# Kernel optimization log

Measured on AMD Instinct MI355X. Metric: run time of the kernel, lower is better.

Reference implementation:

```python
import jax, jax.numpy as jnp
import numpy as np

DIM = 3072
HEADS = 24
HD = 128
FF = 4 * DIM
EPS = 1e-6
SCALE_SHIFT = 1.0


def _ln(x):
    # LayerNorm, elementwise_affine=False
    mu = jnp.mean(x, axis=-1, keepdims=True)
    var = jnp.mean(jnp.square(x - mu), axis=-1, keepdims=True)
    return (x - mu) * jax.lax.rsqrt(var + EPS)


def _rms(x, w):
    # RMSNorm over head_dim with learned weight
    ms = jnp.mean(jnp.square(x), axis=-1, keepdims=True)
    return x * jax.lax.rsqrt(ms + EPS) * w


def _rope(x, cos, sin):
    # x: [B,S,H,D], cos/sin: [S,D]; interleaved rotate-half (diffusers style)
    xr = x.reshape(*x.shape[:-1], -1, 2)
    x1, x2 = xr[..., 0], xr[..., 1]
    rot = jnp.stack([-x2, x1], axis=-1).reshape(x.shape)
    return x * cos[None, :, None, :] + rot * sin[None, :, None, :]


def _mod_params(temb, w, b):
    m = jax.nn.silu(temb) @ w + b  # [B, 6*DIM]
    B = m.shape[0]
    m = m.reshape(B, -1, 6).transpose(0, 2, 1).reshape(B, -1)  # reorder to 6 blocks of DIM
    return jnp.split(m, 2, axis=-1)  # mod1, mod2 each [B, 3*DIM]


def _modulate(x, mp):
    shift, scale, gate = jnp.split(mp, 3, axis=-1)
    scale = scale + SCALE_SHIFT
    return x * scale[:, None, :] + shift[:, None, :], gate[:, None, :]


def setup_inputs() -> dict:
    key = jax.random.key(0)
    ks = jax.random.split(key, 32)
    B, ST, SI = 1, 512, 1024
    S = ST + SI
    r = lambda k, shp, s=1.0: jax.random.normal(k, shp, dtype=jnp.float32) * s
    W = 0.02  # weight init scale
    ang = jax.random.uniform(ks[5], (S, HD), minval=0.0, maxval=2 * np.pi)
    inp = {
        "hidden_states": r(ks[0], (B, SI, DIM)),
        "encoder_hidden_states": r(ks[1], (B, ST, DIM)),
        "encoder_hidden_states_mask": jnp.ones((B, ST), jnp.float32),
        "temb": r(ks[2], (B, DIM)),
        "rope_cos": jnp.cos(ang),
        "rope_sin": jnp.sin(ang),
        "w_img_mod": r(ks[6], (DIM, 6 * DIM), W), "b_img_mod": r(ks[7], (6 * DIM,), W),
        "w_txt_mod": r(ks[8], (DIM, 6 * DIM), W), "b_txt_mod": r(ks[9], (6 * DIM,), W),
        "norm_q_w": jnp.ones((HD,), jnp.float32), "norm_k_w": jnp.ones((HD,), jnp.float32),
        "norm_added_q_w": jnp.ones((HD,), jnp.float32), "norm_added_k_w": jnp.ones((HD,), jnp.float32),
        "w_qkv": r(ks[10], (DIM, 3 * DIM), W), "b_qkv": r(ks[11], (3 * DIM,), W),
        "w_add_qkv": r(ks[12], (DIM, 3 * DIM), W), "b_add_qkv": r(ks[13], (3 * DIM,), W),
        "w_out": r(ks[14], (DIM, DIM), W), "b_out": r(ks[15], (DIM,), W),
        "w_add_out": r(ks[16], (DIM, DIM), W), "b_add_out": r(ks[17], (DIM,), W),
        "w_img_mlp1": r(ks[18], (DIM, FF), W), "b_img_mlp1": r(ks[19], (FF,), W),
        "w_img_mlp2": r(ks[20], (FF, DIM), W), "b_img_mlp2": r(ks[21], (DIM,), W),
        "w_txt_mlp1": r(ks[22], (DIM, FF), W), "b_txt_mlp1": r(ks[23], (FF,), W),
        "w_txt_mlp2": r(ks[24], (FF, DIM), W), "b_txt_mlp2": r(ks[25], (DIM,), W),
    }
    return inp


def reference(hidden_states, encoder_hidden_states, encoder_hidden_states_mask, temb,
              rope_cos, rope_sin,
              w_img_mod, b_img_mod, w_txt_mod, b_txt_mod,
              norm_q_w, norm_k_w, norm_added_q_w, norm_added_k_w,
              w_qkv, b_qkv, w_add_qkv, b_add_qkv,
              w_out, b_out, w_add_out, b_add_out,
              w_img_mlp1, b_img_mlp1, w_img_mlp2, b_img_mlp2,
              w_txt_mlp1, b_txt_mlp1, w_txt_mlp2, b_txt_mlp2):
    B, SI, _ = hidden_states.shape
    ST = encoder_hidden_states.shape[1]

    img_mod1, img_mod2 = _mod_params(temb, w_img_mod, b_img_mod)
    txt_mod1, txt_mod2 = _mod_params(temb, w_txt_mod, b_txt_mod)

    img_m, img_g1 = _modulate(_ln(hidden_states), img_mod1)
    txt_m, txt_g1 = _modulate(_ln(encoder_hidden_states), txt_mod1)

    # joint attention
    iq, ik, iv = jnp.split(img_m @ w_qkv + b_qkv, 3, axis=-1)
    tq, tk, tv = jnp.split(txt_m @ w_add_qkv + b_add_qkv, 3, axis=-1)
    iq = _rms(iq.reshape(B, SI, HEADS, HD), norm_q_w)
    ik = _rms(ik.reshape(B, SI, HEADS, HD), norm_k_w)
    iv = iv.reshape(B, SI, HEADS, HD)
    tq = _rms(tq.reshape(B, ST, HEADS, HD), norm_added_q_w)
    tk = _rms(tk.reshape(B, ST, HEADS, HD), norm_added_k_w)
    tv = tv.reshape(B, ST, HEADS, HD)
    q = jnp.concatenate([tq, iq], axis=1)  # [B,S,H,D], txt first
    k = jnp.concatenate([tk, ik], axis=1)
    v = jnp.concatenate([tv, iv], axis=1)
    q = _rope(q, rope_cos, rope_sin)
    k = _rope(k, rope_cos, rope_sin)
    scores = jnp.einsum('bqhd,bkhd->bhqk', q, k) / np.float32(np.sqrt(HD))
    probs = jax.nn.softmax(scores, axis=-1)
    attn = jnp.einsum('bhqk,bkhd->bqhd', probs, v).reshape(B, ST + SI, HEADS * HD)

    txt_a = attn[:, :ST] @ w_add_out + b_add_out
    img_a = attn[:, ST:] @ w_out + b_out
    hidden = hidden_states + img_g1 * img_a
    enc = encoder_hidden_states + txt_g1 * txt_a

    # fused GELU(tanh) MLPs with modulation
    img_m2, img_g2 = _modulate(_ln(hidden), img_mod2)
    img_mlp = jax.nn.gelu(img_m2 @ w_img_mlp1 + b_img_mlp1, approximate=True) @ w_img_mlp2 + b_img_mlp2
    hidden = hidden + img_g2 * img_mlp

    txt_m2, txt_g2 = _modulate(_ln(enc), txt_mod2)
    txt_mlp = jax.nn.gelu(txt_m2 @ w_txt_mlp1 + b_txt_mlp1, approximate=True) @ w_txt_mlp2 + b_txt_mlp2
    enc = enc + txt_g2 * txt_mlp

    return enc, hidden
```

## Files before the change

kernel.cpp:

```cpp
#include <hip/hip_runtime.h>

#define DIMX 3072
#define STX 512
#define SIX 1024
#define SQX 1536
#define FFX 12288

typedef __attribute__((ext_vector_type(4))) float f32x4;
typedef __attribute__((ext_vector_type(8))) __bf16 bf16x8;
typedef __attribute__((ext_vector_type(4))) int i32x4;

__device__ __forceinline__ unsigned short f2bf(float f){
  unsigned u = __builtin_bit_cast(unsigned, f);
  u += 0x7FFFu + ((u>>16)&1u);
  return (unsigned short)(u>>16);
}
__device__ __forceinline__ float bf2f(unsigned short h){
  unsigned u = ((unsigned)h)<<16;
  return __builtin_bit_cast(float, u);
}
__device__ __forceinline__ float gelu_tanh(float x){
  float x3 = x*x*x;
  float z = 0.7978845608028654f*(x + 0.044715f*x3);
  z = fminf(fmaxf(z, -15.f), 15.f);
  float e = exp2f(z*2.8853900817779268f);
  float th = (e-1.f)/(e+1.f);
  return 0.5f*x*(1.f+th);
}

__device__ __forceinline__ void gload16(const void* g, void* l){
  __builtin_amdgcn_global_load_lds(
      (const __attribute__((address_space(1))) void*)g,
      (__attribute__((address_space(3))) void*)l,
      16, 0, 0);
}


__global__ void k_silu(const float* __restrict__ temb, float* __restrict__ out){
  int i = blockIdx.x*256 + threadIdx.x;
  if(i < DIMX){
    float x = temb[i];
    out[i] = x / (1.f + exp2f(-x*1.4426950408889634f));
  }
}

__global__ void k_modinit(const float* __restrict__ b_img, const float* __restrict__ b_txt,
                          float* __restrict__ mod){
  int idx = blockIdx.x*256 + threadIdx.x;
  int mat = idx / 18432; int r = idx % 18432;
  int i = r/6, j = r%6;
  const float* b = mat ? b_txt : b_img;
  mod[mat*18432 + j*3072 + i] = b[r];
}

__global__ void k_modgemv(const float* __restrict__ w_img, const float* __restrict__ w_txt,
                          const float* __restrict__ silu_t, float* __restrict__ mod){
  int bz = blockIdx.x;
  int ks = bz & 7; bz >>= 3;
  int nc = bz % 18; int mat = bz / 18;
  const float* W = mat ? w_txt : w_img;
  __shared__ float st[384];
  int k0 = ks*384;
  for(int i = threadIdx.x; i < 384; i += 256) st[i] = silu_t[k0+i];
  __syncthreads();
  int n0 = nc*1024 + threadIdx.x*4;
  float ax=0.f, ay=0.f, az=0.f, aw=0.f;
  const float* Wp = W + (size_t)k0*18432 + n0;
  #pragma unroll 4
  for(int k=0;k<384;k++){
    float4 w = *(const float4*)(Wp + (size_t)k*18432);
    float s = st[k];
    ax += s*w.x; ay += s*w.y; az += s*w.z; aw += s*w.w;
  }
  float* md = mod + mat*18432;
  float vals[4] = {ax, ay, az, aw};
  #pragma unroll
  for(int j=0;j<4;j++){
    int n = n0+j; int i = n/6, jj = n%6;
    atomicAdd(&md[jj*3072 + i], vals[j]);
  }
}

__global__ void k_initC(float* __restrict__ out, const float* __restrict__ res,
                        const float* __restrict__ gate, const float* __restrict__ bias){
  int i = (blockIdx.x*256 + threadIdx.x)*4;
  int col = i % 3072;
  float4 r = *(const float4*)(res + i);
  float4 g = *(const float4*)(gate + col);
  float4 b = *(const float4*)(bias + col);
  float4 o = {r.x + g.x*b.x, r.y + g.y*b.y, r.z + g.z*b.z, r.w + g.w*b.w};
  *(float4*)(out + i) = o;
}

__global__ void k_f2b(const float* __restrict__ x, unsigned short* __restrict__ y, int n4){
  int i = blockIdx.x*256 + threadIdx.x;
  if(i < n4){
    float4 v = *(const float4*)(x + (size_t)i*4);
    unsigned short h0 = f2bf(v.x), h1 = f2bf(v.y), h2 = f2bf(v.z), h3 = f2bf(v.w);
    unsigned long long pk = (unsigned long long)(h0 | ((unsigned)h1<<16))
                          | ((unsigned long long)(h2 | ((unsigned)h3<<16))<<32);
    *(unsigned long long*)(y + (size_t)i*4) = pk;
  }
}

__global__ void k_lnmod(const float* __restrict__ x, const float* __restrict__ modp,
                        unsigned short* __restrict__ out){
  int row = blockIdx.x, t = threadIdx.x;
  const float* xr = x + (size_t)row*DIMX;
  float4 v0 = *(const float4*)(xr + t*4);
  float4 v1 = *(const float4*)(xr + 1024 + t*4);
  float4 v2 = *(const float4*)(xr + 2048 + t*4);
  float s  = v0.x+v0.y+v0.z+v0.w + v1.x+v1.y+v1.z+v1.w + v2.x+v2.y+v2.z+v2.w;
  float s2 = v0.x*v0.x+v0.y*v0.y+v0.z*v0.z+v0.w*v0.w
           + v1.x*v1.x+v1.y*v1.y+v1.z*v1.z+v1.w*v1.w
           + v2.x*v2.x+v2.y*v2.y+v2.z*v2.z+v2.w*v2.w;
  #pragma unroll
  for(int o=32;o>0;o>>=1){ s += __shfl_xor(s,o); s2 += __shfl_xor(s2,o); }
  __shared__ float rs_[4], rs2_[4];
  int wid = t>>6;
  if((t&63)==0){ rs_[wid]=s; rs2_[wid]=s2; }
  __syncthreads();
  float S  = rs_[0]+rs_[1]+rs_[2]+rs_[3];
  float S2 = rs2_[0]+rs2_[1]+rs2_[2]+rs2_[3];
  float mu = S*(1.f/3072.f);
  float var = S2*(1.f/3072.f) - mu*mu;
  float rstd = rsqrtf(var + 1e-6f);
  #pragma unroll
  for(int j=0;j<3;j++){
    int c = j*1024 + t*4;
    float4 sh = *(const float4*)(modp + c);
    float4 sc = *(const float4*)(modp + 3072 + c);
    float4 xv = (j==0)?v0:((j==1)?v1:v2);
    unsigned short h0 = f2bf((xv.x-mu)*rstd*(sc.x+1.f)+sh.x);
    unsigned short h1 = f2bf((xv.y-mu)*rstd*(sc.y+1.f)+sh.y);
    unsigned short h2 = f2bf((xv.z-mu)*rstd*(sc.z+1.f)+sh.z);
    unsigned short h3 = f2bf((xv.w-mu)*rstd*(sc.w+1.f)+sh.w);
    unsigned long long pk = (unsigned long long)(h0 | ((unsigned)h1<<16))
                          | ((unsigned long long)(h2 | ((unsigned)h3<<16))<<32);
    *(unsigned long long*)(out + (size_t)row*DIMX + c) = pk;
  }
}

__global__ void k_rmsrope(const unsigned short* __restrict__ qkv_txt,
                          const unsigned short* __restrict__ qkv_img,
                          const float* __restrict__ nqw, const float* __restrict__ nkw,
                          const float* __restrict__ naqw, const float* __restrict__ nakw,
                          const float* __restrict__ cosb, const float* __restrict__ sinb,
                          unsigned short* __restrict__ Q, unsigned short* __restrict__ K,
                          unsigned short* __restrict__ V){
  int s = blockIdx.x, h = blockIdx.y, t = threadIdx.x;
  bool txt = s < STX;
  const unsigned short* src = txt ? (qkv_txt + (size_t)s*9216)
                                  : (qkv_img + (size_t)(s-STX)*9216);
  const float* qw = txt ? naqw : nqw;
  const float* kw = txt ? nakw : nkw;
  int d0 = 2*t;
  float q1 = bf2f(src[h*128 + d0]),        q2 = bf2f(src[h*128 + d0 + 1]);
  float k1 = bf2f(src[3072 + h*128 + d0]), k2 = bf2f(src[3072 + h*128 + d0 + 1]);
  float v1 = bf2f(src[6144 + h*128 + d0]), v2 = bf2f(src[6144 + h*128 + d0 + 1]);
  float sq = q1*q1 + q2*q2, sk = k1*k1 + k2*k2;
  #pragma unroll
  for(int o=32;o>0;o>>=1){ sq += __shfl_xor(sq,o); sk += __shfl_xor(sk,o); }
  float rq = rsqrtf(sq*(1.f/128.f) + 1e-6f);
  float rk = rsqrtf(sk*(1.f/128.f) + 1e-6f);
  q1 *= rq*qw[d0]; q2 *= rq*qw[d0+1];
  k1 *= rk*kw[d0]; k2 *= rk*kw[d0+1];
  float c1 = cosb[(size_t)s*128 + d0], c2 = cosb[(size_t)s*128 + d0 + 1];
  float s1 = sinb[(size_t)s*128 + d0], s2 = sinb[(size_t)s*128 + d0 + 1];
  float Q1 = q1*c1 - q2*s1, Q2 = q2*c2 + q1*s2;
  float K1 = k1*c1 - k2*s1, K2 = k2*c2 + k1*s2;
  size_t o = ((size_t)s*24 + h)*128 + d0;
  Q[o] = f2bf(Q1); Q[o+1] = f2bf(Q2);
  K[o] = f2bf(K1); K[o+1] = f2bf(K2);
  V[o] = f2bf(v1); V[o+1] = f2bf(v2);
}

__global__ void k_vtrans(const unsigned short* __restrict__ V, unsigned short* __restrict__ VT){
  __shared__ unsigned short tile[64][136];
  int st = blockIdx.x, h = blockIdx.y, t = threadIdx.x;
  int s0 = st*64;
  {
    int s = t>>2;
    #pragma unroll
    for(int i=0;i<4;i++){
      int oct = ((t&3)<<2) + i;
      i32x4 d = *(const i32x4*)(V + ((size_t)(s0+s)*24 + h)*128 + oct*8);
      *(i32x4*)&tile[s][oct*8] = d;
    }
  }
  __syncthreads();
  {
    int d0 = t>>3; int strip = t&7;
    #pragma unroll
    for(int i=0;i<4;i++){
      int d = d0 + i*32;
      unsigned short h8[8];
      #pragma unroll
      for(int j=0;j<8;j++) h8[j] = tile[strip*8 + j][d];
      unsigned a0 = h8[0] | ((unsigned)h8[1]<<16);
      unsigned a1 = h8[2] | ((unsigned)h8[3]<<16);
      unsigned a2 = h8[4] | ((unsigned)h8[5]<<16);
      unsigned a3 = h8[6] | ((unsigned)h8[7]<<16);
      i32x4 dv = {(int)a0,(int)a1,(int)a2,(int)a3};
      *(i32x4*)(VT + ((size_t)h*128 + d)*1536 + s0 + strip*8) = dv;
    }
  }
}

__global__ void k_softmax(unsigned short* __restrict__ S){
  size_t row = blockIdx.x;
  unsigned short* p = S + row*1536;
  int t = threadIdx.x;
  float v[6];
  float m = -1e30f;
  #pragma unroll
  for(int j=0;j<6;j++){ v[j] = bf2f(p[t + j*256]); m = fmaxf(m, v[j]); }
  #pragma unroll
  for(int o=32;o>0;o>>=1) m = fmaxf(m, __shfl_xor(m, o));
  __shared__ float red[4];
  int wid = t>>6;
  if((t&63)==0) red[wid] = m;
  __syncthreads();
  float M = fmaxf(fmaxf(red[0],red[1]), fmaxf(red[2],red[3]));
  __syncthreads();
  float s = 0.f;
  #pragma unroll
  for(int j=0;j<6;j++){ v[j] = exp2f((v[j]-M)*1.4426950408889634f); s += v[j]; }
  #pragma unroll
  for(int o=32;o>0;o>>=1) s += __shfl_xor(s, o);
  if((t&63)==0) red[wid] = s;
  __syncthreads();
  float inv = 1.f/(red[0]+red[1]+red[2]+red[3]);
  #pragma unroll
  for(int j=0;j<6;j++) p[t + j*256] = f2bf(v[j]*inv);
}

__global__ __launch_bounds__(256,4) void k_gemm(
    const unsigned short* __restrict__ A, long lda, long sAz,
    const unsigned short* __restrict__ BT, long ldb, long sBz,
    const float* __restrict__ bias,
    void* __restrict__ Cp, long ldc, long sCz,
    int K, int KS, int mode, float alpha,
    const float* __restrict__ gate)
{
  __shared__ unsigned short Als[128*32];
  __shared__ unsigned short Bls[128*32];
  const int t = threadIdx.x;
  const int bn = blockIdx.x, bm = blockIdx.y;
  const int z = blockIdx.z, zh = z / KS, zs = z - zh*KS;
  const int Kc = K / KS, kbeg = zs*Kc, kend = kbeg + Kc;

  const unsigned short* Ab = A  + (size_t)zh*sAz + (size_t)bm*128*lda;
  const unsigned short* Bb = BT + (size_t)zh*sBz + (size_t)bn*128*ldb;

  const int lane = t & 63, wid = t>>6, wr = wid>>1, wc = wid&1;
  const int lr = lane & 15, lk = lane>>4;
  const int srow = (lane>>2);
  const int soff = (lane&3)*8;

  f32x4 acc[4][4];
  #pragma unroll
  for(int i=0;i<4;i++)
    #pragma unroll
    for(int j=0;j<4;j++) acc[i][j] = {0.f,0.f,0.f,0.f};

  for(int k0=kbeg; k0<kend; k0+=32){
    __syncthreads();
    gload16(Ab + (size_t)(     wid*16 + srow)*lda + k0 + soff, Als + (     wid*16)*32);
    gload16(Ab + (size_t)(64 + wid*16 + srow)*lda + k0 + soff, Als + (64 + wid*16)*32);
    gload16(Bb + (size_t)(     wid*16 + srow)*ldb + k0 + soff, Bls + (     wid*16)*32);
    gload16(Bb + (size_t)(64 + wid*16 + srow)*ldb + k0 + soff, Bls + (64 + wid*16)*32);
    __syncthreads();
    bf16x8 af[4], bfr[4];
    #pragma unroll
    for(int mf=0;mf<4;mf++) af[mf]  = *(const bf16x8*)&Als[(wr*64 + mf*16 + lr)*32 + lk*8];
    #pragma unroll
    for(int nf=0;nf<4;nf++) bfr[nf] = *(const bf16x8*)&Bls[(wc*64 + nf*16 + lr)*32 + lk*8];
    #pragma unroll
    for(int mf=0;mf<4;mf++)
      #pragma unroll
      for(int nf=0;nf<4;nf++)
        acc[mf][nf] = __builtin_amdgcn_mfma_f32_16x16x32_bf16(af[mf], bfr[nf], acc[mf][nf], 0,0,0);
  }

  unsigned short* C16 = (unsigned short*)Cp + (size_t)zh*sCz;
  float* C32 = (float*)Cp + (size_t)zh*sCz;
  #pragma unroll
  for(int mf=0;mf<4;mf++){
    #pragma unroll
    for(int nf=0;nf<4;nf++){
      #pragma unroll
      for(int r=0;r<4;r++){
        size_t row = (size_t)bm*128 + wr*64 + mf*16 + lk*4 + r;
        size_t col = (size_t)bn*128 + wc*64 + nf*16 + lr;
        float v = acc[mf][nf][r]*alpha;
        if(mode==0){
          C16[row*ldc + col] = f2bf(v + (bias ? bias[col] : 0.f));
        } else if(mode==1){
          C16[row*ldc + col] = f2bf(gelu_tanh(v + (bias ? bias[col] : 0.f)));
        } else {
          float g = gate ? gate[col] : 1.f;
          atomicAdd(&C32[row*ldc + col], g*v);
        }
      }
    }
  }
}

__global__ __launch_bounds__(256,4) void k_gemmW(
    const unsigned short* __restrict__ A, long lda,
    const float* __restrict__ W, long ldw,
    const float* __restrict__ bias,
    void* __restrict__ Cp, long ldc,
    int K, int KS, int mode,
    const float* __restrict__ gate)
{
  __shared__ unsigned short Als[128*32];
  __shared__ float BlsW[32*128];
  const int t = threadIdx.x;
  const int bn = blockIdx.x, bm = blockIdx.y;
  const int zs = blockIdx.z;
  const int Kc = K / KS, kbeg = zs*Kc, kend = kbeg + Kc;

  const unsigned short* Ab = A + (size_t)bm*128*lda;
  const float* Wb = W + (size_t)bn*128;

  const int lane = t & 63, wid = t>>6, wr = wid>>1, wc = wid&1;
  const int lr = lane & 15, lk = lane>>4;
  const int srow = (lane>>2);
  const int soff = (lane&3)*8;
  const int wrow = (lane>>5);
  const int wcol = (lane&31)*4;

  f32x4 acc[4][4];
  #pragma unroll
  for(int i=0;i<4;i++)
    #pragma unroll
    for(int j=0;j<4;j++) acc[i][j] = {0.f,0.f,0.f,0.f};

  for(int k0=kbeg; k0<kend; k0+=32){
    __syncthreads();
    gload16(Ab + (size_t)(     wid*16 + srow)*lda + k0 + soff, Als + (     wid*16)*32);
    gload16(Ab + (size_t)(64 + wid*16 + srow)*lda + k0 + soff, Als + (64 + wid*16)*32);
    #pragma unroll
    for(int i=0;i<4;i++){
      int r0 = wid*8 + i*2;
      gload16(Wb + (size_t)(k0 + r0 + wrow)*ldw + wcol, BlsW + r0*128);
    }
    __syncthreads();
    bf16x8 af[4], bfr[4];
    #pragma unroll
    for(int mf=0;mf<4;mf++) af[mf] = *(const bf16x8*)&Als[(wr*64 + mf*16 + lr)*32 + lk*8];
    #pragma unroll
    for(int nf=0;nf<4;nf++){
      const float* Bcol = BlsW + lk*8*128 + wc*64 + nf*16 + lr;
      bf16x8 bv;
      #pragma unroll
      for(int j=0;j<8;j++) bv[j] = (__bf16)Bcol[j*128];
      bfr[nf] = bv;
    }
    #pragma unroll
    for(int mf=0;mf<4;mf++)
      #pragma unroll
      for(int nf=0;nf<4;nf++)
        acc[mf][nf] = __builtin_amdgcn_mfma_f32_16x16x32_bf16(af[mf], bfr[nf], acc[mf][nf], 0,0,0);
  }

  unsigned short* C16 = (unsigned short*)Cp;
  float* C32 = (float*)Cp;
  #pragma unroll
  for(int mf=0;mf<4;mf++){
    #pragma unroll
    for(int nf=0;nf<4;nf++){
      #pragma unroll
      for(int r=0;r<4;r++){
        size_t row = (size_t)bm*128 + wr*64 + mf*16 + lk*4 + r;
        size_t col = (size_t)bn*128 + wc*64 + nf*16 + lr;
        float v = acc[mf][nf][r];
        if(mode==0){
          C16[row*ldc + col] = f2bf(v + (bias ? bias[col] : 0.f));
        } else if(mode==1){
          C16[row*ldc + col] = f2bf(gelu_tanh(v + (bias ? bias[col] : 0.f)));
        } else {
          float g = gate ? gate[col] : 1.f;
          atomicAdd(&C32[row*ldc + col], g*v);
        }
      }
    }
  }
}


extern "C" void kernel_launch(void* const* d_in, const int* in_sizes, int n_in,
                              void* d_out, int out_size, void* d_ws, size_t ws_size,
                              hipStream_t stream){
  const float* hidden_states = (const float*)d_in[0];
  const float* enc_states    = (const float*)d_in[1];
  const float* temb          = (const float*)d_in[3];
  const float* rope_cos      = (const float*)d_in[4];
  const float* rope_sin      = (const float*)d_in[5];
  const float* w_img_mod     = (const float*)d_in[6];
  const float* b_img_mod     = (const float*)d_in[7];
  const float* w_txt_mod     = (const float*)d_in[8];
  const float* b_txt_mod     = (const float*)d_in[9];
  const float* norm_q_w      = (const float*)d_in[10];
  const float* norm_k_w      = (const float*)d_in[11];
  const float* norm_aq_w     = (const float*)d_in[12];
  const float* norm_ak_w     = (const float*)d_in[13];
  const float* w_qkv   = (const float*)d_in[14];
  const float* b_qkv   = (const float*)d_in[15];
  const float* w_aqkv  = (const float*)d_in[16];
  const float* b_aqkv  = (const float*)d_in[17];
  const float* w_out_  = (const float*)d_in[18];
  const float* b_out_  = (const float*)d_in[19];
  const float* w_aout  = (const float*)d_in[20];
  const float* b_aout  = (const float*)d_in[21];
  const float* w_mlp1i = (const float*)d_in[22];
  const float* b_mlp1i = (const float*)d_in[23];
  const float* w_mlp2i = (const float*)d_in[24];
  const float* b_mlp2i = (const float*)d_in[25];
  const float* w_mlp1t = (const float*)d_in[26];
  const float* b_mlp1t = (const float*)d_in[27];
  const float* w_mlp2t = (const float*)d_in[28];
  const float* b_mlp2t = (const float*)d_in[29];

  char* ws = (char*)d_ws;
  float* mod    = (float*)(ws + 0);
  float* silu_t = (float*)(ws + 147456);
  unsigned short* imgm = (unsigned short*)(ws + 159744);
  unsigned short* txtm = (unsigned short*)(ws + 6451200);
  float* hid = (float*)(ws + 9596928);
  float* enc = (float*)(ws + 22179840);
  float* attnf = (float*)(ws + 28471296);
  unsigned short* Qb  = (unsigned short*)(ws + 47345664);
  unsigned short* Kb  = (unsigned short*)(ws + 56782848);
  unsigned short* Vb  = (unsigned short*)(ws + 66220032);
  unsigned short* attnb = (unsigned short*)(ws + 66220032);
  unsigned short* VTb = (unsigned short*)(ws + 75657216);
  unsigned short* Sbuf = (unsigned short*)(ws + 85094400);
  unsigned short* qkvi = (unsigned short*)(ws + 141717504);
  unsigned short* qkvt = (unsigned short*)(ws + 160591872);
  unsigned short* mlph = (unsigned short*)(ws + 103968768);

  float* out_enc = (float*)d_out;
  float* out_hid = (float*)d_out + (size_t)STX*DIMX;

  k_silu<<<12,256,0,stream>>>(temb, silu_t);
  k_modinit<<<144,256,0,stream>>>(b_img_mod, b_txt_mod, mod);
  k_modgemv<<<288,256,0,stream>>>(w_img_mod, w_txt_mod, silu_t, mod);

  k_lnmod<<<SIX,256,0,stream>>>(hidden_states, mod + 0,     imgm);
  k_lnmod<<<STX,256,0,stream>>>(enc_states,    mod + 18432, txtm);

  k_gemmW<<<dim3(72,8,1),256,0,stream>>>(imgm,3072, w_qkv,9216, b_qkv,
      qkvi,9216, 3072,1, 0, nullptr);
  k_gemmW<<<dim3(72,4,1),256,0,stream>>>(txtm,3072, w_aqkv,9216, b_aqkv,
      qkvt,9216, 3072,1, 0, nullptr);

  k_rmsrope<<<dim3(1536,24),64,0,stream>>>(qkvt, qkvi, norm_q_w, norm_k_w,
      norm_aq_w, norm_ak_w, rope_cos, rope_sin, Qb, Kb, Vb);
  k_vtrans<<<dim3(24,24),256,0,stream>>>(Vb, VTb);

  hipMemsetAsync(attnf, 0, (size_t)1536*3072*4, stream);
  for(int g=0; g<3; g++){
    long hb = g*8;
    k_gemm<<<dim3(12,12,8),256,0,stream>>>(Qb + hb*128, 3072, 128,
        Kb + hb*128, 3072, 128, nullptr,
        Sbuf, 1536, (long)1536*1536, 128,1, 0, 0.08838834764831845f, nullptr);
    k_softmax<<<8*1536,256,0,stream>>>(Sbuf);
    k_gemm<<<dim3(1,12,32),256,0,stream>>>(Sbuf, 1536, (long)1536*1536,
        VTb + (size_t)hb*128*1536, 1536, (long)128*1536, nullptr,
        attnf + hb*128, 3072, 128, 1536,4, 3, 1.f, nullptr);
  }
  k_f2b<<<4608,256,0,stream>>>(attnf, attnb, 1536*3072/4);

  k_initC<<<512*3,256,0,stream>>>(enc, enc_states, mod + 18432 + 2*3072, b_aout);
  k_initC<<<1024*3,256,0,stream>>>(hid, hidden_states, mod + 2*3072, b_out_);
  k_gemmW<<<dim3(24,4,4),256,0,stream>>>(attnb,3072, w_aout,3072, nullptr,
      enc,3072, 3072,4, 3, mod + 18432 + 2*3072);
  k_gemmW<<<dim3(24,8,4),256,0,stream>>>(attnb + (size_t)512*3072,3072, w_out_,3072, nullptr,
      hid,3072, 3072,4, 3, mod + 2*3072);

  k_lnmod<<<SIX,256,0,stream>>>(hid, mod + 3*3072, imgm);
  k_gemmW<<<dim3(96,8,1),256,0,stream>>>(imgm,3072, w_mlp1i,12288, b_mlp1i,
      mlph,12288, 3072,1, 1, nullptr);
  k_initC<<<1024*3,256,0,stream>>>(out_hid, hid, mod + 5*3072, b_mlp2i);
  k_gemmW<<<dim3(24,8,4),256,0,stream>>>(mlph,12288, w_mlp2i,3072, nullptr,
      out_hid,3072, 12288,4, 3, mod + 5*3072);

  k_lnmod<<<STX,256,0,stream>>>(enc, mod + 18432 + 3*3072, txtm);
  k_gemmW<<<dim3(96,4,1),256,0,stream>>>(txtm,3072, w_mlp1t,12288, b_mlp1t,
      mlph,12288, 3072,1, 1, nullptr);
  k_initC<<<512*3,256,0,stream>>>(out_enc, enc, mod + 18432 + 5*3072, b_mlp2t);
  k_gemmW<<<dim3(24,4,8),256,0,stream>>>(mlph,12288, w_mlp2t,3072, nullptr,
      out_enc,3072, 12288,8, 3, mod + 18432 + 5*3072);
}
```

Baseline: 1.372 ms.

## Fuse attention into flash-attention kernel and stage weight bf16 conversion in LDS

Replaces the three-group pipeline of QK^T GEMM, a separate softmax pass over a materialized score buffer, split-K PV GEMM with fp32 atomics and a final fp32-to-bf16 conversion with one online-softmax flash-attention kernel that writes bf16 output directly. This removes the large score-buffer round trips, the memset and the atomics. Separately, the fp32-weight GEMM now converts the weight tile to bf16 once into a padded transposed LDS buffer, instead of doing strided per-element conversions for each fragment. It also raises split-K for the text out-projection. The trade-off is an extra LDS pass and barrier per K step, and lower occupancy for the attention kernel, whose 288-block grid may not fill the GPU.

```diff
diff --git a/kernel.cpp b/kernel.cpp
--- a/kernel.cpp
+++ b/kernel.cpp
@@ -9,11 +9,15 @@
 typedef __attribute__((ext_vector_type(4))) float f32x4;
 typedef __attribute__((ext_vector_type(8))) __bf16 bf16x8;
 typedef __attribute__((ext_vector_type(4))) int i32x4;
+typedef __attribute__((ext_vector_type(4))) unsigned short u16x4;
 
 __device__ __forceinline__ unsigned short f2bf(float f){
   unsigned u = __builtin_bit_cast(unsigned, f);
   u += 0x7FFFu + ((u>>16)&1u);
   return (unsigned short)(u>>16);
+}
+__device__ __forceinline__ unsigned short usbf(float x){
+  return __builtin_bit_cast(unsigned short, (__bf16)x);
 }
 __device__ __forceinline__ float bf2f(unsigned short h){
   unsigned u = ((unsigned)h)<<16;
@@ -92,17 +96,6 @@
   *(float4*)(out + i) = o;
 }
 
-__global__ void k_f2b(const float* __restrict__ x, unsigned short* __restrict__ y, int n4){
-  int i = blockIdx.x*256 + threadIdx.x;
-  if(i < n4){
-    float4 v = *(const float4*)(x + (size_t)i*4);
-    unsigned short h0 = f2bf(v.x), h1 = f2bf(v.y), h2 = f2bf(v.z), h3 = f2bf(v.w);
-    unsigned long long pk = (unsigned long long)(h0 | ((unsigned)h1<<16))
-                          | ((unsigned long long)(h2 | ((unsigned)h3<<16))<<32);
-    *(unsigned long long*)(y + (size_t)i*4) = pk;
-  }
-}
-
 __global__ void k_lnmod(const float* __restrict__ x, const float* __restrict__ modp,
                         unsigned short* __restrict__ out){
   int row = blockIdx.x, t = threadIdx.x;
@@ -207,101 +200,138 @@
   }
 }
 
-__global__ void k_softmax(unsigned short* __restrict__ S){
-  size_t row = blockIdx.x;
-  unsigned short* p = S + row*1536;
-  int t = threadIdx.x;
-  float v[6];
-  float m = -1e30f;
-  #pragma unroll
-  for(int j=0;j<6;j++){ v[j] = bf2f(p[t + j*256]); m = fmaxf(m, v[j]); }
-  #pragma unroll
-  for(int o=32;o>0;o>>=1) m = fmaxf(m, __shfl_xor(m, o));
-  __shared__ float red[4];
-  int wid = t>>6;
-  if((t&63)==0) red[wid] = m;
-  __syncthreads();
-  float M = fmaxf(fmaxf(red[0],red[1]), fmaxf(red[2],red[3]));
-  __syncthreads();
-  float s = 0.f;
-  #pragma unroll
-  for(int j=0;j<6;j++){ v[j] = exp2f((v[j]-M)*1.4426950408889634f); s += v[j]; }
-  #pragma unroll
-  for(int o=32;o>0;o>>=1) s += __shfl_xor(s, o);
-  if((t&63)==0) red[wid] = s;
-  __syncthreads();
-  float inv = 1.f/(red[0]+red[1]+red[2]+red[3]);
-  #pragma unroll
-  for(int j=0;j<6;j++) p[t + j*256] = f2bf(v[j]*inv);
-}
-
-__global__ __launch_bounds__(256,4) void k_gemm(
-    const unsigned short* __restrict__ A, long lda, long sAz,
-    const unsigned short* __restrict__ BT, long ldb, long sBz,
-    const float* __restrict__ bias,
-    void* __restrict__ Cp, long ldc, long sCz,
-    int K, int KS, int mode, float alpha,
-    const float* __restrict__ gate)
+__global__ __launch_bounds__(256,2) void k_fattn(
+    const unsigned short* __restrict__ Q,
+    const unsigned short* __restrict__ Kb,
+    const unsigned short* __restrict__ VT,
+    unsigned short* __restrict__ O)
 {
-  __shared__ unsigned short Als[128*32];
-  __shared__ unsigned short Bls[128*32];
+  __shared__ unsigned short Kls[4][64][32];
+  __shared__ unsigned short Vls[2][128][32];
+  __shared__ unsigned short Pls[128][72];
   const int t = threadIdx.x;
-  const int bn = blockIdx.x, bm = blockIdx.y;
-  const int z = blockIdx.z, zh = z / KS, zs = z - zh*KS;
-  const int Kc = K / KS, kbeg = zs*Kc, kend = kbeg + Kc;
-
-  const unsigned short* Ab = A  + (size_t)zh*sAz + (size_t)bm*128*lda;
-  const unsigned short* Bb = BT + (size_t)zh*sBz + (size_t)bn*128*ldb;
-
-  const int lane = t & 63, wid = t>>6, wr = wid>>1, wc = wid&1;
-  const int lr = lane & 15, lk = lane>>4;
-  const int srow = (lane>>2);
-  const int soff = (lane&3)*8;
-
-  f32x4 acc[4][4];
-  #pragma unroll
-  for(int i=0;i<4;i++)
-    #pragma unroll
-    for(int j=0;j<4;j++) acc[i][j] = {0.f,0.f,0.f,0.f};
-
-  for(int k0=kbeg; k0<kend; k0+=32){
+  const int qb = blockIdx.x, h = blockIdx.y;
+  const int lane = t&63, w = t>>6;
+  const int lr = lane&15, lk = lane>>4;
+  const float SC  = 0.08838834764831845f;
+  const float L2E = 1.4426950408889634f;
+
+  bf16x8 qf[2][4];
+  {
+    const unsigned short* qp = Q + ((size_t)(qb*128 + w*32 + lr)*3072) + h*128 + lk*8;
+    #pragma unroll
+    for(int mf=0;mf<2;mf++)
+      #pragma unroll
+      for(int ks=0;ks<4;ks++)
+        qf[mf][ks] = *(const bf16x8*)(qp + (size_t)mf*16*3072 + ks*32);
+  }
+
+  f32x4 o[2][8];
+  #pragma unroll
+  for(int i=0;i<2;i++)
+    #pragma unroll
+    for(int j=0;j<8;j++) o[i][j] = (f32x4){0.f,0.f,0.f,0.f};
+  float mrow[2][4], lrow[2][4];
+  #pragma unroll
+  for(int i=0;i<2;i++)
+    #pragma unroll
+    for(int r=0;r<4;r++){ mrow[i][r] = -3.0e30f; lrow[i][r] = 0.f; }
+
+  for(int kv0=0; kv0<SQX; kv0+=64){
     __syncthreads();
-    gload16(Ab + (size_t)(     wid*16 + srow)*lda + k0 + soff, Als + (     wid*16)*32);
-    gload16(Ab + (size_t)(64 + wid*16 + srow)*lda + k0 + soff, Als + (64 + wid*16)*32);
-    gload16(Bb + (size_t)(     wid*16 + srow)*ldb + k0 + soff, Bls + (     wid*16)*32);
-    gload16(Bb + (size_t)(64 + wid*16 + srow)*ldb + k0 + soff, Bls + (64 + wid*16)*32);
+    {
+      const unsigned short* kp = Kb + ((size_t)(kv0 + (lane>>2))*3072) + h*128 + w*32 + (lane&3)*8;
+      #pragma unroll
+      for(int i=0;i<4;i++)
+        gload16(kp + (size_t)i*16*3072, &Kls[w][i*16][0]);
+    }
+    {
+      int c = w>>1;
+      const unsigned short* vp = VT + ((size_t)(h*128 + (w&1)*64 + (lane>>2)))*1536 + kv0 + c*32 + (lane&3)*8;
+      #pragma unroll
+      for(int j=0;j<4;j++)
+        gload16(vp + (size_t)j*16*1536, &Vls[c][(w&1)*64 + j*16][0]);
+    }
     __syncthreads();
-    bf16x8 af[4], bfr[4];
-    #pragma unroll
-    for(int mf=0;mf<4;mf++) af[mf]  = *(const bf16x8*)&Als[(wr*64 + mf*16 + lr)*32 + lk*8];
-    #pragma unroll
-    for(int nf=0;nf<4;nf++) bfr[nf] = *(const bf16x8*)&Bls[(wc*64 + nf*16 + lr)*32 + lk*8];
-    #pragma unroll
-    for(int mf=0;mf<4;mf++)
+
+    f32x4 s[2][4];
+    #pragma unroll
+    for(int mf=0;mf<2;mf++)
+      #pragma unroll
+      for(int nf=0;nf<4;nf++) s[mf][nf] = (f32x4){0.f,0.f,0.f,0.f};
+    #pragma unroll
+    for(int ks=0;ks<4;ks++){
+      bf16x8 kf[4];
+      #pragma unroll
+      for(int nf=0;nf<4;nf++) kf[nf] = *(const bf16x8*)&Kls[ks][nf*16+lr][lk*8];
+      #pragma unroll
+      for(int mf=0;mf<2;mf++)
+        #pragma unroll
+        for(int nf=0;nf<4;nf++)
+          s[mf][nf] = __builtin_amdgcn_mfma_f32_16x16x32_bf16(qf[mf][ks], kf[nf], s[mf][nf], 0,0,0);
+    }
+
+    #pragma unroll
+    for(int mf=0;mf<2;mf++){
+      #pragma unroll
+      for(int r=0;r<4;r++){
+        float v = fmaxf(fmaxf(s[mf][0][r], s[mf][1][r]), fmaxf(s[mf][2][r], s[mf][3][r]));
+        #pragma unroll
+        for(int d=1; d<16; d<<=1) v = fmaxf(v, __shfl_xor(v, d));
+        float nm = fmaxf(mrow[mf][r], v*SC);
+        float fac = exp2f((mrow[mf][r]-nm)*L2E);
+        mrow[mf][r] = nm;
+        float rs = 0.f;
+        #pragma unroll
+        for(int nf=0;nf<4;nf++){
+          float p = exp2f((s[mf][nf][r]*SC - nm)*L2E);
+          s[mf][nf][r] = p;
+          rs += p;
+        }
+        #pragma unroll
+        for(int d=1; d<16; d<<=1) rs += __shfl_xor(rs, d);
+        lrow[mf][r] = lrow[mf][r]*fac + rs;
+        #pragma unroll
+        for(int nf=0;nf<8;nf++) o[mf][nf][r] *= fac;
+      }
+    }
+
+    #pragma unroll
+    for(int mf=0;mf<2;mf++)
       #pragma unroll
       for(int nf=0;nf<4;nf++)
-        acc[mf][nf] = __builtin_amdgcn_mfma_f32_16x16x32_bf16(af[mf], bfr[nf], acc[mf][nf], 0,0,0);
-  }
-
-  unsigned short* C16 = (unsigned short*)Cp + (size_t)zh*sCz;
-  float* C32 = (float*)Cp + (size_t)zh*sCz;
-  #pragma unroll
-  for(int mf=0;mf<4;mf++){
-    #pragma unroll
-    for(int nf=0;nf<4;nf++){
+        #pragma unroll
+        for(int r=0;r<4;r++)
+          Pls[w*32 + mf*16 + lk*4 + r][nf*16 + lr] = usbf(s[mf][nf][r]);
+
+    #pragma unroll
+    for(int ks2=0; ks2<2; ks2++){
+      bf16x8 pa[2];
+      #pragma unroll
+      for(int mf=0;mf<2;mf++)
+        pa[mf] = *(const bf16x8*)&Pls[w*32 + mf*16 + lr][ks2*32 + lk*8];
+      #pragma unroll
+      for(int nf=0;nf<8;nf++){
+        bf16x8 vf = *(const bf16x8*)&Vls[ks2][nf*16+lr][lk*8];
+        #pragma unroll
+        for(int mf=0;mf<2;mf++)
+          o[mf][nf] = __builtin_amdgcn_mfma_f32_16x16x32_bf16(pa[mf], vf, o[mf][nf], 0,0,0);
+      }
+    }
+  }
+
+  #pragma unroll
+  for(int mf=0;mf<2;mf++){
+    float inv[4];
+    #pragma unroll
+    for(int r=0;r<4;r++) inv[r] = 1.f/lrow[mf][r];
+    #pragma unroll
+    for(int nf=0;nf<8;nf++){
       #pragma unroll
       for(int r=0;r<4;r++){
-        size_t row = (size_t)bm*128 + wr*64 + mf*16 + lk*4 + r;
-        size_t col = (size_t)bn*128 + wc*64 + nf*16 + lr;
-        float v = acc[mf][nf][r]*alpha;
-        if(mode==0){
-          C16[row*ldc + col] = f2bf(v + (bias ? bias[col] : 0.f));
-        } else if(mode==1){
-          C16[row*ldc + col] = f2bf(gelu_tanh(v + (bias ? bias[col] : 0.f)));
-        } else {
-          float g = gate ? gate[col] : 1.f;
-          atomicAdd(&C32[row*ldc + col], g*v);
-        }
+        size_t row = (size_t)qb*128 + w*32 + mf*16 + lk*4 + r;
+        size_t col = (size_t)h*128 + nf*16 + lr;
+        O[row*3072 + col] = usbf(o[mf][nf][r]*inv[r]);
       }
     }
   }
@@ -316,7 +346,8 @@
     const float* __restrict__ gate)
 {
   __shared__ unsigned short Als[128*32];
-  __shared__ float BlsW[32*128];
+  __shared__ float Wls[32*128];
+  __shared__ unsigned short Bls[128*40];
   const int t = threadIdx.x;
   const int bn = blockIdx.x, bm = blockIdx.y;
   const int zs = blockIdx.z;
@@ -331,6 +362,8 @@
   const int soff = (lane&3)*8;
   const int wrow = (lane>>5);
   const int wcol = (lane&31)*4;
+  const int ck = (t&7)*4;
+  const int cn = (t>>3)*4;
 
   f32x4 acc[4][4];
   #pragma unroll
@@ -345,20 +378,26 @@
     #pragma unroll
     for(int i=0;i<4;i++){
       int r0 = wid*8 + i*2;
-      gload16(Wb + (size_t)(k0 + r0 + wrow)*ldw + wcol, BlsW + r0*128);
+      gload16(Wb + (size_t)(k0 + r0 + wrow)*ldw + wcol, Wls + r0*128);
+    }
+    __syncthreads();
+    {
+      f32x4 r0 = *(const f32x4*)&Wls[(ck+0)*128 + cn];
+      f32x4 r1 = *(const f32x4*)&Wls[(ck+1)*128 + cn];
+      f32x4 r2 = *(const f32x4*)&Wls[(ck+2)*128 + cn];
+      f32x4 r3 = *(const f32x4*)&Wls[(ck+3)*128 + cn];
+      #pragma unroll
+      for(int jn=0;jn<4;jn++){
+        u16x4 pk = { usbf(r0[jn]), usbf(r1[jn]), usbf(r2[jn]), usbf(r3[jn]) };
+        *(u16x4*)&Bls[(cn+jn)*40 + ck] = pk;
+      }
     }
     __syncthreads();
     bf16x8 af[4], bfr[4];
     #pragma unroll
-    for(int mf=0;mf<4;mf++) af[mf] = *(const bf16x8*)&Als[(wr*64 + mf*16 + lr)*32 + lk*8];
-    #pragma unroll
-    for(int nf=0;nf<4;nf++){
-      const float* Bcol = BlsW + lk*8*128 + wc*64 + nf*16 + lr;
-      bf16x8 bv;
-      #pragma unroll
-      for(int j=0;j<8;j++) bv[j] = (__bf16)Bcol[j*128];
-      bfr[nf] = bv;
-    }
+    for(int mf=0;mf<4;mf++) af[mf]  = *(const bf16x8*)&Als[(wr*64 + mf*16 + lr)*32 + lk*8];
+    #pragma unroll
+    for(int nf=0;nf<4;nf++) bfr[nf] = *(const bf16x8*)&Bls[(wc*64 + nf*16 + lr)*40 + lk*8];
     #pragma unroll
     for(int mf=0;mf<4;mf++)
       #pragma unroll
@@ -431,13 +470,11 @@
   unsigned short* txtm = (unsigned short*)(ws + 6451200);
   float* hid = (float*)(ws + 9596928);
   float* enc = (float*)(ws + 22179840);
-  float* attnf = (float*)(ws + 28471296);
   unsigned short* Qb  = (unsigned short*)(ws + 47345664);
   unsigned short* Kb  = (unsigned short*)(ws + 56782848);
   unsigned short* Vb  = (unsigned short*)(ws + 66220032);
   unsigned short* attnb = (unsigned short*)(ws + 66220032);
   unsigned short* VTb = (unsigned short*)(ws + 75657216);
-  unsigned short* Sbuf = (unsigned short*)(ws + 85094400);
   unsigned short* qkvi = (unsigned short*)(ws + 141717504);
   unsigned short* qkvt = (unsigned short*)(ws + 160591872);
   unsigned short* mlph = (unsigned short*)(ws + 103968768);
@@ -461,23 +498,12 @@
       norm_aq_w, norm_ak_w, rope_cos, rope_sin, Qb, Kb, Vb);
   k_vtrans<<<dim3(24,24),256,0,stream>>>(Vb, VTb);
 
-  hipMemsetAsync(attnf, 0, (size_t)1536*3072*4, stream);
-  for(int g=0; g<3; g++){
-    long hb = g*8;
-    k_gemm<<<dim3(12,12,8),256,0,stream>>>(Qb + hb*128, 3072, 128,
-        Kb + hb*128, 3072, 128, nullptr,
-        Sbuf, 1536, (long)1536*1536, 128,1, 0, 0.08838834764831845f, nullptr);
-    k_softmax<<<8*1536,256,0,stream>>>(Sbuf);
-    k_gemm<<<dim3(1,12,32),256,0,stream>>>(Sbuf, 1536, (long)1536*1536,
-        VTb + (size_t)hb*128*1536, 1536, (long)128*1536, nullptr,
-        attnf + hb*128, 3072, 128, 1536,4, 3, 1.f, nullptr);
-  }
-  k_f2b<<<4608,256,0,stream>>>(attnf, attnb, 1536*3072/4);
+  k_fattn<<<dim3(12,24),256,0,stream>>>(Qb, Kb, VTb, attnb);
 
   k_initC<<<512*3,256,0,stream>>>(enc, enc_states, mod + 18432 + 2*3072, b_aout);
   k_initC<<<1024*3,256,0,stream>>>(hid, hidden_states, mod + 2*3072, b_out_);
-  k_gemmW<<<dim3(24,4,4),256,0,stream>>>(attnb,3072, w_aout,3072, nullptr,
-      enc,3072, 3072,4, 3, mod + 18432 + 2*3072);
+  k_gemmW<<<dim3(24,4,8),256,0,stream>>>(attnb,3072, w_aout,3072, nullptr,
+      enc,3072, 3072,8, 3, mod + 18432 + 2*3072);
   k_gemmW<<<dim3(24,8,4),256,0,stream>>>(attnb + (size_t)512*3072,3072, w_out_,3072, nullptr,
       hid,3072, 3072,4, 3, mod + 2*3072);
 
```

New measurement: 1.251 ms. -8.8%, faster.
